# Optimization experiments

Hardware: AMD Instinct MI355X
Metric: run time of the kernel (lower is better)

Reference implementation:

```python
import jax, jax.numpy as jnp
import numpy as np

LX, LY = 256, 256
K_CLASSES = 4
N_SWEEPS = 2
N_SITES = LX * LY

# 8-neighborhood offsets (Moore neighborhood), border handled by clipping
_OFFSETS = np.array([[-1, -1], [-1, 0], [-1, 1],
                     [0, -1],           [0, 1],
                     [1, -1],  [1, 0],  [1, 1]], dtype=np.int32)


def setup_inputs() -> dict:
    key = jax.random.key(0)
    k1, k2, k3, k4 = jax.random.split(key, 4)
    X_init = jax.random.randint(k1, (LX, LY), 0, K_CLASSES).astype(jnp.int32)
    perm = jax.random.permutation(k2, jnp.arange(N_SITES)).astype(jnp.int32)
    uniforms = jax.random.uniform(k3, (N_SWEEPS, N_SITES), dtype=jnp.float32)
    beta = jax.random.uniform(k4, (), dtype=jnp.float32) + 0.5  # Potts coupling
    return {"X_init": X_init, "perm": perm, "uniforms": uniforms,
            "beta": beta, "K": K_CLASSES}


def reference(X_init, perm, uniforms, beta, K):
    lx, ly = X_init.shape
    off = jnp.asarray(_OFFSETS)              # (8, 2)
    classes = jnp.arange(K)                  # (K,)

    def update_one_site(X, uv, r):
        u, v = jnp.unravel_index(uv, (lx, ly))
        uu = jnp.clip(u + off[:, 0], 0, lx - 1)   # (8,) neighbor rows
        vv = jnp.clip(v + off[:, 1], 0, ly - 1)   # (8,) neighbor cols
        neigh = X[uu, vv]                          # (8,) dynamic gather
        # Potts potential: p_k proportional to exp(beta * #{neighbors == k})
        counts = (neigh[None, :] == classes[:, None]).sum(axis=1)  # (K,)
        probs = jax.nn.softmax(beta * counts.astype(jnp.float32))  # (K,) sums to 1
        # inverse-CDF categorical sample, as in the original cumsum < r
        x_sample = jnp.count_nonzero(jnp.cumsum(probs) < r)
        return X.at[u, v].set(x_sample.astype(X.dtype))  # scatter write

    def one_sweep(X, rs):
        def body(Xc, inp):
            uv, r = inp
            return update_one_site(Xc, uv, r), None
        X, _ = jax.lax.scan(body, X, (perm, rs))
        return X, None

    X_final, _ = jax.lax.scan(one_sweep, X_init, uniforms)  # N_SWEEPS sweeps
    return X_final
```

## Files before the change

### kernel.cpp

```cpp
#include <hip/hip_runtime.h>
#include <math.h>

#define NSITES 65536
#define WIN 4096
#define NW 16
#define RMAX 32


__device__ __forceinline__ int agg_pos(int v, int* c, int vmax) {
  int pos = 0;
  const int lane = threadIdx.x & 63;
  for (int vv = 1; vv <= vmax; ++vv) {
    unsigned long long m = __ballot(v == vv);
    if (m) {
      int leader = __ffsll((long long)m) - 1;
      int base = 0;
      if (lane == leader) base = atomicAdd(&c[vv], (int)__popcll(m));
      base = __shfl(base, leader);
      if (v == vv) pos = base + (int)__popcll(m & ((1ull << lane) - 1ull));
    }
  }
  return pos;
}

__device__ __forceinline__ void do_update(unsigned char* cell,
                                          const unsigned int* cellw,
                                          const float2* ct01,
                                          const float2* ct23, unsigned uvv,
                                          float r) {
  const int u = uvv >> 8, v = (int)(uvv & 255u);
  const int um = u ? u - 1 : 0, up = u < 255 ? u + 1 : 255;
  const int vm = v ? v - 1 : 0, vp = v < 255 ? v + 1 : 255;
  const int cb = vm >> 2;
  const int sh0 = (vm & 3) << 3;
  const int shv = (v - vm) << 3;
  const int shp = (vp - vm) << 3;
  int acc = 0;
  {
    const unsigned int* rw = cellw + (um << 6) + cb;
    const unsigned long long wd =
        ((unsigned long long)rw[1] << 32) | (unsigned long long)rw[0];
    const unsigned wl = (unsigned)(wd >> sh0);
    acc += 1 << ((wl & 255u) << 2);
    acc += 1 << (((wl >> shv) & 255u) << 2);
    acc += 1 << (((wl >> shp) & 255u) << 2);
  }
  {
    const unsigned int* rw = cellw + (u << 6) + cb;
    const unsigned long long wd =
        ((unsigned long long)rw[1] << 32) | (unsigned long long)rw[0];
    const unsigned wl = (unsigned)(wd >> sh0);
    acc += 1 << ((wl & 255u) << 2);
    acc += 1 << (((wl >> shp) & 255u) << 2);
  }
  {
    const unsigned int* rw = cellw + (up << 6) + cb;
    const unsigned long long wd =
        ((unsigned long long)rw[1] << 32) | (unsigned long long)rw[0];
    const unsigned wl = (unsigned)(wd >> sh0);
    acc += 1 << ((wl & 255u) << 2);
    acc += 1 << (((wl >> shv) & 255u) << 2);
    acc += 1 << (((wl >> shp) & 255u) << 2);
  }
  const int n0 = acc & 15, n1 = (acc >> 4) & 15, n2 = (acc >> 8) & 15;
  const int idx = n0 + 9 * n1 + 81 * n2;
  const float2 a = ct01[idx];
  const float2 b = ct23[idx];
  int cnt = (a.x < r) ? 1 : 0;
  cnt += (a.y < r) ? 1 : 0;
  cnt += (b.x < r) ? 1 : 0;
  cnt += (b.y < r) ? 1 : 0;
  cell[uvv] = (unsigned char)cnt;
}

__device__ __forceinline__ void run_rounds(unsigned char* cell,
                                           const unsigned int* cellw,
                                           const float2* ct01,
                                           const float2* ct23, const int* le,
                                           const uint2 (&R)[4], int tid) {
  int b = 0, e = le[1];
  for (int rd = 1; rd < RMAX; ++rd) {
    if (b >= WIN) break;
    const int nb = e;
    const int ne = (rd + 1 < RMAX) ? le[rd + 1] : e;
#pragma unroll
    for (int k = 0; k < 4; ++k) {
      const int s = tid + (k << 10);
      if (s >= b && s < e)
        do_update(cell, cellw, ct01, ct23, R[k].x, __uint_as_float(R[k].y));
    }
    __syncthreads();
    b = nb;
    e = ne;
  }
}

__global__ __launch_bounds__(1024) void GibbsSampler_90443421319469_kernel(
    const int* __restrict__ Xi, const int* __restrict__ perm,
    const float* __restrict__ uni, const float* __restrict__ betap,
    uint2* __restrict__ recpk, int* __restrict__ ends,
    int* __restrict__ flag, int* __restrict__ out) {
#pragma clang fp contract(off)
  __shared__ __align__(16) unsigned char smem[139552];
  unsigned short* posg = (unsigned short*)smem;
  unsigned short* lvl = (unsigned short*)(smem + 131072);
  int* cnt = (int*)(smem + 139264);
  int* coff = (int*)(smem + 139396);
  int* bmax = (int*)(smem + 139532);
  unsigned int* cellw = (unsigned int*)smem;
  float2* ct01 = (float2*)(smem + 65536);
  float2* ct23 = (float2*)(smem + 71424);
  int* lend = (int*)(smem + 77312);

  const int tid = threadIdx.x;

  if (blockIdx.x != 0) {
    const int w = blockIdx.x - 1;
    const int wbase = w * WIN;

    for (int g = tid; g < NSITES / 8; g += 1024)
      ((uint4*)posg)[g] = make_uint4(0u, 0u, 0u, 0u);
    for (int i = tid; i <= RMAX; i += 1024) { cnt[i] = 0; coff[i] = 0; }
    if (tid == 0) *bmax = 0;
    __syncthreads();

    int uvk[4];
#pragma unroll
    for (int k = 0; k < 4; ++k) {
      const int lt = tid + k * 1024;
      uvk[k] = perm[wbase + lt];
      posg[uvk[k]] = (unsigned short)(lt + 1);
    }
    __syncthreads();

    unsigned short pred[4][8];
    int myl[4];
#pragma unroll
    for (int k = 0; k < 4; ++k) {
      const int lt = tid + k * 1024;
      const int uv = uvk[k], u = uv >> 8, v = uv & 255;
      const int um = u ? u - 1 : 0, up = u < 255 ? u + 1 : 255;
      const int vm = v ? v - 1 : 0, vp = v < 255 ? v + 1 : 255;
      const int nb8[8] = {(um << 8) | vm, (um << 8) | v, (um << 8) | vp,
                          (u << 8) | vm,                 (u << 8) | vp,
                          (up << 8) | vm, (up << 8) | v, (up << 8) | vp};
      bool hasp = false;
#pragma unroll
      for (int j = 0; j < 8; ++j) {
        const int p = posg[nb8[j]];
        pred[k][j] = (p && p - 1 < lt) ? (unsigned short)(p - 1)
                                       : (unsigned short)0xFFFF;
        hasp |= (pred[k][j] != (unsigned short)0xFFFF);
      }
      myl[k] = hasp ? 2 : 1;
      lvl[lt] = (unsigned short)myl[k];
    }
    __syncthreads();

    for (int pass = 1; pass < 128; ++pass) {
      bool ch = false;
#pragma unroll
      for (int k = 0; k < 4; ++k) {
        if (myl[k] > pass) {
          int m = 0;
#pragma unroll
          for (int j = 0; j < 8; ++j) {
            const unsigned short p = pred[k][j];
            if (p != 0xFFFF) m = max(m, (int)lvl[p]);
          }
          const int nl = m + 1;
          if (nl != myl[k]) {
            myl[k] = nl;
            lvl[tid + k * 1024] = (unsigned short)nl;
            ch = true;
          }
        }
      }
      if (__syncthreads_count((int)ch) == 0) break;
    }

#pragma unroll
    for (int k = 0; k < 4; ++k) atomicMax(bmax, myl[k]);
    __syncthreads();
    const int vmax = *bmax;

#pragma unroll
    for (int k = 0; k < 4; ++k) (void)agg_pos(myl[k], cnt, vmax);
    __syncthreads();
    if (tid == 0) {
      int e = 0;
      for (int r = 0; r < RMAX; ++r) {
        coff[r] = e;
        e += cnt[r];
        ends[w * RMAX + r] = e;
      }
    }
    __syncthreads();

#pragma unroll
    for (int k = 0; k < 4; ++k) {
      const int pos = agg_pos(myl[k], coff, vmax);
      const int lt = tid + k * 1024;
      const int gp = wbase + pos;
      recpk[gp] = make_uint2((unsigned)uvk[k],
                             __float_as_uint(uni[wbase + lt]));
      recpk[NSITES + gp] =
          make_uint2((unsigned)uvk[k],
                     __float_as_uint(uni[NSITES + wbase + lt]));
    }
    __syncthreads();
    if (tid == 0) {
      __threadfence();
      atomicAdd(flag, 1);
    }
    return;
  }

  unsigned char* cell = (unsigned char*)cellw;
  const float beta = betap[0];

  for (int g = tid; g < NSITES / 4; g += 1024) {
    int4 x = ((const int4*)Xi)[g];
    cellw[g] = (unsigned)(x.x & 255) | ((unsigned)(x.y & 255) << 8) |
               ((unsigned)(x.z & 255) << 16) | ((unsigned)(x.w & 255) << 24);
  }
  for (int t = tid; t < 729; t += 1024) {
    const int n0 = t % 9, n1 = (t / 9) % 9, n2 = t / 81;
    const int n3 = 8 - n0 - n1 - n2;
    float4 val = make_float4(2.f, 2.f, 2.f, 2.f);
    if (n3 >= 0) {
      const int mx = max(max(n0, n1), max(n2, n3));
      const float xm = beta * (float)mx;
      const float x0 = beta * (float)n0;
      const float x1 = beta * (float)n1;
      const float x2 = beta * (float)n2;
      const float x3 = beta * (float)n3;
      const float e0 = (float)exp((double)(x0 - xm));
      const float e1 = (float)exp((double)(x1 - xm));
      const float e2 = (float)exp((double)(x2 - xm));
      const float e3 = (float)exp((double)(x3 - xm));
      const float s = ((e0 + e1) + e2) + e3;
      const float c0 = e0 / s;
      const float c1 = c0 + e1 / s;
      const float c2 = c1 + e2 / s;
      const float c3 = c2 + e3 / s;
      val = make_float4(c0, c1, c2, c3);
    }
    ct01[t] = make_float2(val.x, val.y);
    ct23[t] = make_float2(val.z, val.w);
  }

  if (tid == 0) {
    while (__hip_atomic_load(flag, __ATOMIC_RELAXED,
                             __HIP_MEMORY_SCOPE_AGENT) < NW)
      __builtin_amdgcn_s_sleep(2);
    __threadfence();
  }
  __syncthreads();

  uint2 ra[4], rb[4];
#pragma unroll
  for (int k = 0; k < 4; ++k) ra[k] = recpk[tid + (k << 10)];
  if (tid < NW * RMAX) lend[tid] = ends[tid];
  __syncthreads();

  for (int ww2 = 0; ww2 < 2 * NW; ++ww2) {
    const int ww = ww2 & (NW - 1);
    const int* le = &lend[ww * RMAX];
    const int wn = ww2 + 1;
    const uint2* rpn = recpk + (wn >> 4) * NSITES + (wn & (NW - 1)) * WIN;
    if ((ww2 & 1) == 0) {
      if (wn < 2 * NW) {
#pragma unroll
        for (int k = 0; k < 4; ++k) rb[k] = rpn[tid + (k << 10)];
      }
      run_rounds(cell, cellw, ct01, ct23, le, ra, tid);
    } else {
      if (wn < 2 * NW) {
#pragma unroll
        for (int k = 0; k < 4; ++k) ra[k] = rpn[tid + (k << 10)];
      }
      run_rounds(cell, cellw, ct01, ct23, le, rb, tid);
    }
  }

  for (int g = tid; g < NSITES / 4; g += 1024) {
    const unsigned p = cellw[g];
    int4 o;
    o.x = (int)(p & 255u);
    o.y = (int)((p >> 8) & 255u);
    o.z = (int)((p >> 16) & 255u);
    o.w = (int)((p >> 24) & 255u);
    ((int4*)out)[g] = o;
  }
}

extern "C" void kernel_launch(void* const* d_in, const int* in_sizes, int n_in,
                              void* d_out, int out_size, void* d_ws,
                              size_t ws_size, hipStream_t stream) {
  const int* Xi = (const int*)d_in[0];
  const int* perm = (const int*)d_in[1];
  const float* uni = (const float*)d_in[2];
  const float* beta = (const float*)d_in[3];
  int* out = (int*)d_out;

  char* ws = (char*)d_ws;
  uint2* recpk = (uint2*)ws;
  int* ends = (int*)(ws + 2 * NSITES * 8);
  int* flag = (int*)(ws + 2 * NSITES * 8 + NW * RMAX * 4);

  hipMemsetAsync(flag, 0, sizeof(int), stream);
  GibbsSampler_90443421319469_kernel<<<dim3(NW + 1), dim3(1024), 0, stream>>>(
      Xi, perm, uni, beta, recpk, ends, flag, out);
}
```

Measured before the change: 210.8 us.

## Replace level-scheduled rounds with dataflow spin-wait on per-site done flags

Removes the helper blocks' iterative level computation and per-round compaction. Each site now carries an 8-bit mask of earlier neighbours in its window. The main block spins on per-site epoch flags in shared memory and updates a site once all of its predecessors are marked done. This replaces one __syncthreads per dependency level with fine-grained spinning inside a window, but it risks wavefront divergence, busy-wait stalls inside a wave, and a guard-based exit that could skip updates.

```diff
diff --git a/kernel.cpp b/kernel.cpp
--- a/kernel.cpp
+++ b/kernel.cpp
@@ -4,31 +4,14 @@
 #define NSITES 65536
 #define WIN 4096
 #define NW 16
-#define RMAX 32
-
-
-__device__ __forceinline__ int agg_pos(int v, int* c, int vmax) {
-  int pos = 0;
-  const int lane = threadIdx.x & 63;
-  for (int vv = 1; vv <= vmax; ++vv) {
-    unsigned long long m = __ballot(v == vv);
-    if (m) {
-      int leader = __ffsll((long long)m) - 1;
-      int base = 0;
-      if (lane == leader) base = atomicAdd(&c[vv], (int)__popcll(m));
-      base = __shfl(base, leader);
-      if (v == vv) pos = base + (int)__popcll(m & ((1ull << lane) - 1ull));
-    }
-  }
-  return pos;
-}
+
 
 __device__ __forceinline__ void do_update(unsigned char* cell,
                                           const unsigned int* cellw,
                                           const float2* ct01,
-                                          const float2* ct23, unsigned uvv,
+                                          const float2* ct23, unsigned site,
                                           float r) {
-  const int u = uvv >> 8, v = (int)(uvv & 255u);
+  const int u = (int)(site >> 8), v = (int)(site & 255u);
   const int um = u ? u - 1 : 0, up = u < 255 ? u + 1 : 255;
   const int vm = v ? v - 1 : 0, vp = v < 255 ? v + 1 : 255;
   const int cb = vm >> 2;
@@ -70,47 +53,69 @@
   cnt += (a.y < r) ? 1 : 0;
   cnt += (b.x < r) ? 1 : 0;
   cnt += (b.y < r) ? 1 : 0;
-  cell[uvv] = (unsigned char)cnt;
-}
-
-__device__ __forceinline__ void run_rounds(unsigned char* cell,
-                                           const unsigned int* cellw,
-                                           const float2* ct01,
-                                           const float2* ct23, const int* le,
-                                           const uint2 (&R)[4], int tid) {
-  int b = 0, e = le[1];
-  for (int rd = 1; rd < RMAX; ++rd) {
-    if (b >= WIN) break;
-    const int nb = e;
-    const int ne = (rd + 1 < RMAX) ? le[rd + 1] : e;
+  cell[site] = (unsigned char)cnt;
+}
+
+__device__ __forceinline__ void run_flow(unsigned char* cell,
+                                         const unsigned int* cellw,
+                                         const float2* ct01,
+                                         const float2* ct23,
+                                         volatile unsigned char* vdone,
+                                         unsigned char* done, int epoch,
+                                         const uint2 (&R)[4]) {
+  unsigned site_[4], rem_[4];
+  int pend = 0;
+#pragma unroll
+  for (int k = 0; k < 4; ++k) {
+    site_[k] = R[k].x & 0xFFFFu;
+    rem_[k] = (R[k].x >> 16) & 255u;
+    pend |= 1 << k;
+  }
+  int guard = 0;
+  while (pend) {
 #pragma unroll
     for (int k = 0; k < 4; ++k) {
-      const int s = tid + (k << 10);
-      if (s >= b && s < e)
-        do_update(cell, cellw, ct01, ct23, R[k].x, __uint_as_float(R[k].y));
-    }
-    __syncthreads();
-    b = nb;
-    e = ne;
+      if (!(pend & (1 << k))) continue;
+      unsigned rem = rem_[k];
+      if (rem) {
+        const int u = (int)(site_[k] >> 8), v = (int)(site_[k] & 255u);
+        const int um = u ? u - 1 : 0, up = u < 255 ? u + 1 : 255;
+        const int vm = v ? v - 1 : 0, vp = v < 255 ? v + 1 : 255;
+        const int nb8[8] = {(um << 8) | vm, (um << 8) | v, (um << 8) | vp,
+                            (u << 8) | vm,                 (u << 8) | vp,
+                            (up << 8) | vm, (up << 8) | v, (up << 8) | vp};
+#pragma unroll
+        for (int j = 0; j < 8; ++j) {
+          if (rem & (1u << j)) {
+            if ((int)vdone[nb8[j]] == epoch) rem &= ~(1u << j);
+          }
+        }
+        rem_[k] = rem;
+      }
+      if (rem == 0) {
+        asm volatile("" ::: "memory");
+        do_update(cell, cellw, ct01, ct23, site_[k], __uint_as_float(R[k].y));
+        asm volatile("s_waitcnt lgkmcnt(0)" ::: "memory");
+        done[site_[k]] = (unsigned char)epoch;
+        pend &= ~(1 << k);
+      }
+    }
+    if (++guard > (1 << 16)) break;
   }
 }
 
 __global__ __launch_bounds__(1024) void GibbsSampler_90443421319469_kernel(
     const int* __restrict__ Xi, const int* __restrict__ perm,
     const float* __restrict__ uni, const float* __restrict__ betap,
-    uint2* __restrict__ recpk, int* __restrict__ ends,
-    int* __restrict__ flag, int* __restrict__ out) {
+    uint2* __restrict__ recpk, int* __restrict__ flag,
+    int* __restrict__ out) {
 #pragma clang fp contract(off)
-  __shared__ __align__(16) unsigned char smem[139552];
+  __shared__ __align__(16) unsigned char smem[142848];
   unsigned short* posg = (unsigned short*)smem;
-  unsigned short* lvl = (unsigned short*)(smem + 131072);
-  int* cnt = (int*)(smem + 139264);
-  int* coff = (int*)(smem + 139396);
-  int* bmax = (int*)(smem + 139532);
   unsigned int* cellw = (unsigned int*)smem;
   float2* ct01 = (float2*)(smem + 65536);
   float2* ct23 = (float2*)(smem + 71424);
-  int* lend = (int*)(smem + 77312);
+  unsigned char* done = smem + 77312;
 
   const int tid = threadIdx.x;
 
@@ -120,8 +125,6 @@
 
     for (int g = tid; g < NSITES / 8; g += 1024)
       ((uint4*)posg)[g] = make_uint4(0u, 0u, 0u, 0u);
-    for (int i = tid; i <= RMAX; i += 1024) { cnt[i] = 0; coff[i] = 0; }
-    if (tid == 0) *bmax = 0;
     __syncthreads();
 
     int uvk[4];
@@ -133,8 +136,6 @@
     }
     __syncthreads();
 
-    unsigned short pred[4][8];
-    int myl[4];
 #pragma unroll
     for (int k = 0; k < 4; ++k) {
       const int lt = tid + k * 1024;
@@ -144,69 +145,17 @@
       const int nb8[8] = {(um << 8) | vm, (um << 8) | v, (um << 8) | vp,
                           (u << 8) | vm,                 (u << 8) | vp,
                           (up << 8) | vm, (up << 8) | v, (up << 8) | vp};
-      bool hasp = false;
+      unsigned mask = 0;
 #pragma unroll
       for (int j = 0; j < 8; ++j) {
         const int p = posg[nb8[j]];
-        pred[k][j] = (p && p - 1 < lt) ? (unsigned short)(p - 1)
-                                       : (unsigned short)0xFFFF;
-        hasp |= (pred[k][j] != (unsigned short)0xFFFF);
-      }
-      myl[k] = hasp ? 2 : 1;
-      lvl[lt] = (unsigned short)myl[k];
-    }
-    __syncthreads();
-
-    for (int pass = 1; pass < 128; ++pass) {
-      bool ch = false;
-#pragma unroll
-      for (int k = 0; k < 4; ++k) {
-        if (myl[k] > pass) {
-          int m = 0;
-#pragma unroll
-          for (int j = 0; j < 8; ++j) {
-            const unsigned short p = pred[k][j];
-            if (p != 0xFFFF) m = max(m, (int)lvl[p]);
-          }
-          const int nl = m + 1;
-          if (nl != myl[k]) {
-            myl[k] = nl;
-            lvl[tid + k * 1024] = (unsigned short)nl;
-            ch = true;
-          }
-        }
-      }
-      if (__syncthreads_count((int)ch) == 0) break;
-    }
-
-#pragma unroll
-    for (int k = 0; k < 4; ++k) atomicMax(bmax, myl[k]);
-    __syncthreads();
-    const int vmax = *bmax;
-
-#pragma unroll
-    for (int k = 0; k < 4; ++k) (void)agg_pos(myl[k], cnt, vmax);
-    __syncthreads();
-    if (tid == 0) {
-      int e = 0;
-      for (int r = 0; r < RMAX; ++r) {
-        coff[r] = e;
-        e += cnt[r];
-        ends[w * RMAX + r] = e;
-      }
-    }
-    __syncthreads();
-
-#pragma unroll
-    for (int k = 0; k < 4; ++k) {
-      const int pos = agg_pos(myl[k], coff, vmax);
-      const int lt = tid + k * 1024;
-      const int gp = wbase + pos;
-      recpk[gp] = make_uint2((unsigned)uvk[k],
-                             __float_as_uint(uni[wbase + lt]));
-      recpk[NSITES + gp] =
-          make_uint2((unsigned)uvk[k],
-                     __float_as_uint(uni[NSITES + wbase + lt]));
+        if (p && p - 1 < lt) mask |= 1u << j;
+      }
+      const unsigned ux = (unsigned)uv | (mask << 16);
+      recpk[wbase + lt] =
+          make_uint2(ux, __float_as_uint(uni[wbase + lt]));
+      recpk[NSITES + wbase + lt] =
+          make_uint2(ux, __float_as_uint(uni[NSITES + wbase + lt]));
     }
     __syncthreads();
     if (tid == 0) {
@@ -224,6 +173,8 @@
     cellw[g] = (unsigned)(x.x & 255) | ((unsigned)(x.y & 255) << 8) |
                ((unsigned)(x.z & 255) << 16) | ((unsigned)(x.w & 255) << 24);
   }
+  for (int g = tid; g < NSITES / 16; g += 1024)
+    ((uint4*)done)[g] = make_uint4(0u, 0u, 0u, 0u);
   for (int t = tid; t < 729; t += 1024) {
     const int n0 = t % 9, n1 = (t / 9) % 9, n2 = t / 81;
     const int n3 = 8 - n0 - n1 - n2;
@@ -258,15 +209,14 @@
   }
   __syncthreads();
 
+  volatile unsigned char* vdone = done;
+
   uint2 ra[4], rb[4];
 #pragma unroll
   for (int k = 0; k < 4; ++k) ra[k] = recpk[tid + (k << 10)];
-  if (tid < NW * RMAX) lend[tid] = ends[tid];
-  __syncthreads();
 
   for (int ww2 = 0; ww2 < 2 * NW; ++ww2) {
-    const int ww = ww2 & (NW - 1);
-    const int* le = &lend[ww * RMAX];
+    const int epoch = ww2 + 1;
     const int wn = ww2 + 1;
     const uint2* rpn = recpk + (wn >> 4) * NSITES + (wn & (NW - 1)) * WIN;
     if ((ww2 & 1) == 0) {
@@ -274,14 +224,15 @@
 #pragma unroll
         for (int k = 0; k < 4; ++k) rb[k] = rpn[tid + (k << 10)];
       }
-      run_rounds(cell, cellw, ct01, ct23, le, ra, tid);
+      run_flow(cell, cellw, ct01, ct23, vdone, done, epoch, ra);
     } else {
       if (wn < 2 * NW) {
 #pragma unroll
         for (int k = 0; k < 4; ++k) ra[k] = rpn[tid + (k << 10)];
       }
-      run_rounds(cell, cellw, ct01, ct23, le, rb, tid);
-    }
+      run_flow(cell, cellw, ct01, ct23, vdone, done, epoch, rb);
+    }
+    __syncthreads();
   }
 
   for (int g = tid; g < NSITES / 4; g += 1024) {
@@ -306,10 +257,9 @@
 
   char* ws = (char*)d_ws;
   uint2* recpk = (uint2*)ws;
-  int* ends = (int*)(ws + 2 * NSITES * 8);
-  int* flag = (int*)(ws + 2 * NSITES * 8 + NW * RMAX * 4);
+  int* flag = (int*)(ws + 2 * NSITES * 8);
 
   hipMemsetAsync(flag, 0, sizeof(int), stream);
   GibbsSampler_90443421319469_kernel<<<dim3(NW + 1), dim3(1024), 0, stream>>>(
-      Xi, perm, uni, beta, recpk, ends, flag, out);
-}
+      Xi, perm, uni, beta, recpk, flag, out);
+}
```

After: 374.5 us. +77.7%, slower.
